# Optimization experiments

Hardware: AMD Instinct MI355X
Metric: run time of the kernel (lower is better)

Reference implementation:

```python
import jax, jax.numpy as jnp
import numpy as np

PRUNING_RATE = 0.1
ROPE_THETA = 10000.0
EPS = 1e-5


def _rms_norm(x, w):
    v = jnp.mean(jnp.square(x.astype(jnp.float32)), axis=-1, keepdims=True)
    return (x * jax.lax.rsqrt(v + EPS)).astype(x.dtype) * w


def _rotate_half(x):
    x1, x2 = jnp.split(x, 2, axis=-1)
    return jnp.concatenate([-x2, x1], axis=-1)


def setup_inputs() -> dict:
    key = jax.random.key(0)
    ks = jax.random.split(key, 11)
    B, Q, D, H, Dh, P, F = 2, 16, 2048, 16, 128, 8192, 5632
    K = P + Q
    s = D ** -0.5
    inp = {
        "hidden_states": jax.random.normal(ks[0], (B, Q, D), jnp.float32),
        "past_k": jax.random.normal(ks[1], (B, H, P, Dh), jnp.float32),
        "past_v": jax.random.normal(ks[2], (B, H, P, Dh), jnp.float32),
        "wq": jax.random.normal(ks[3], (D, D), jnp.float32) * s,
        "wk": jax.random.normal(ks[4], (D, D), jnp.float32) * s,
        "wv": jax.random.normal(ks[5], (D, D), jnp.float32) * s,
        "wo": jax.random.normal(ks[6], (D, D), jnp.float32) * s,
        "w_gate": jax.random.normal(ks[7], (D, F), jnp.float32) * s,
        "w_up": jax.random.normal(ks[8], (D, F), jnp.float32) * s,
        "w_down": jax.random.normal(ks[9], (F, D), jnp.float32) * (F ** -0.5),
        "norm1_w": jnp.ones((D,), jnp.float32),
        "norm2_w": jnp.ones((D,), jnp.float32),
    }
    # causal mask over [past + new] keys: query i (global pos P+i) sees keys <= P+i
    q_pos = P + jnp.arange(Q)
    k_pos = jnp.arange(K)
    mask = jnp.where(k_pos[None, :] <= q_pos[:, None], 0.0, -1e9).astype(jnp.float32)
    inp["attn_mask"] = jnp.broadcast_to(mask[None, None], (B, 1, Q, K))
    return inp


def reference(hidden_states, past_k, past_v, attn_mask, wq, wk, wv, wo,
              w_gate, w_up, w_down, norm1_w, norm2_w):
    B, Q, D = hidden_states.shape
    _, H, P, Dh = past_k.shape
    K = P + Q

    residual = hidden_states
    x = _rms_norm(hidden_states, norm1_w)
    q = (x @ wq).reshape(B, Q, H, Dh).transpose(0, 2, 1, 3)  # [B,H,Q,Dh]
    k = (x @ wk).reshape(B, Q, H, Dh).transpose(0, 2, 1, 3)
    v = (x @ wv).reshape(B, Q, H, Dh).transpose(0, 2, 1, 3)

    # RoPE at cache positions P..P+Q-1 (past keys already rotated)
    inv_freq = 1.0 / (ROPE_THETA ** (jnp.arange(0, Dh, 2, dtype=jnp.float32) / Dh))
    pos = (P + jnp.arange(Q)).astype(jnp.float32)
    emb = jnp.concatenate([pos[:, None] * inv_freq[None, :]] * 2, axis=-1)  # [Q,Dh]
    cos, sin = jnp.cos(emb), jnp.sin(emb)
    q = q * cos + _rotate_half(q) * sin
    k = k * cos + _rotate_half(k) * sin

    k_full = jnp.concatenate([past_k, k], axis=2)  # [B,H,K,Dh]
    v_full = jnp.concatenate([past_v, v], axis=2)

    scores = jnp.einsum("bhqd,bhkd->bhqk", q, k_full) / jnp.sqrt(jnp.float32(Dh))
    scores = scores + attn_mask
    attn = jax.nn.softmax(scores, axis=-1)  # eager weights (output_attentions=True)
    out = jnp.einsum("bhqk,bhkd->bhqd", attn, v_full)
    out = out.transpose(0, 2, 1, 3).reshape(B, Q, D) @ wo
    h = residual + out

    y = _rms_norm(h, norm2_w)
    new_hidden = h + (jax.nn.silu(y @ w_gate) * (y @ w_up)) @ w_down

    # importance-based KV eviction: mean attn to last query over batch*heads
    imp = jnp.sum(attn[:, :, Q - 1, :], axis=(0, 1)) / (B * H)  # [K]
    imp = imp.at[K - 1].set(jnp.inf)  # never evict the last token's key
    n_prune = int(PRUNING_RATE * K)
    _, prune_idxs = jax.lax.top_k(-imp, n_prune)  # smallest-importance keys
    return new_hidden, attn, prune_idxs
```

## Files before the change

### kernel.cpp

```cpp
#include <hip/hip_runtime.h>
#include <math.h>

#define BB 2
#define QQ 16
#define DD 2048
#define HH 16
#define DHH 128
#define PP 8192
#define FF 5632
#define KK 8208
#define BH 32
#define RR 32
#define NPRUNE 820

#define OFF_X      0u
#define OFF_QR     65536u
#define OFF_KN     131072u
#define OFF_VN     196608u
#define OFF_ROWM   262144u
#define OFF_ROWZ   262656u
#define OFF_OATTN  263168u
#define OFF_H      328704u
#define OFF_Y      394240u
#define OFF_ACT    459776u
#define OFF_UNION  640064u
#define OFF_P64P   (OFF_UNION + 12582912u)
#define OFF_F64    (OFF_P64P + 4456448u)
#define D_X64      0u
#define D_K64      65536u
#define D_Q64      131072u
#define D_M64      135168u
#define D_Z64      135200u
#define D_SC       135232u
#define D_KEYS     397888u
#define OFF_RANK   (OFF_F64 + 812192u)

__global__ __launch_bounds__(256) void rmsnorm_kernel(
    const float* __restrict__ in, const float* __restrict__ w,
    float* __restrict__ out)
{
    int r = blockIdx.x;
    const float* x = in + (size_t)r * DD;
    float ss = 0.f;
    for (int c = threadIdx.x; c < DD; c += 256) { float v = x[c]; ss = fmaf(v, v, ss); }
    __shared__ float red[256];
    red[threadIdx.x] = ss;
    __syncthreads();
    for (int off = 128; off > 0; off >>= 1) {
        if (threadIdx.x < off) red[threadIdx.x] += red[threadIdx.x + off];
        __syncthreads();
    }
    float mean = red[0] / (float)DD;
    float scale = 1.0f / sqrtf(mean + 1e-5f);
    for (int c = threadIdx.x; c < DD; c += 256)
        out[(size_t)r * DD + c] = x[c] * scale * w[c];
}

__global__ __launch_bounds__(256) void fused_rms_kernel(
    const float* __restrict__ in, const float* __restrict__ w,
    float* __restrict__ out32, double* __restrict__ out64)
{
    int bx = blockIdx.x, tid = threadIdx.x;
    __shared__ float red[256];
    __shared__ float bs[16];
    __shared__ float sscale;
    if (bx < 32) {
        int r = bx;
        const float* x = in + (size_t)r * DD;
        float ss = 0.f;
        for (int c = tid; c < DD; c += 256) { float v = x[c]; ss = fmaf(v, v, ss); }
        red[tid] = ss;
        __syncthreads();
        for (int off = 128; off > 0; off >>= 1) {
            if (tid < off) red[tid] += red[tid + off];
            __syncthreads();
        }
        float mean = red[0] / (float)DD;
        float scale = 1.0f / sqrtf(mean + 1e-5f);
        for (int c = tid; c < DD; c += 256)
            out32[(size_t)r * DD + c] = x[c] * scale * w[c];
    } else {
        int r = bx - 32;
        const float* x = in + (size_t)r * DD;
        if (tid < 16) {
            const float* a = x + tid * 128;
            float rr[8];
#pragma unroll
            for (int j = 0; j < 8; ++j) { float v = a[j]; rr[j] = __fmul_rn(v, v); }
            for (int i = 8; i < 128; i += 8) {
#pragma unroll
                for (int j = 0; j < 8; ++j) {
                    float v = a[i + j];
                    rr[j] = __fadd_rn(rr[j], __fmul_rn(v, v));
                }
            }
            float t01 = __fadd_rn(rr[0], rr[1]);
            float t23 = __fadd_rn(rr[2], rr[3]);
            float t45 = __fadd_rn(rr[4], rr[5]);
            float t67 = __fadd_rn(rr[6], rr[7]);
            bs[tid] = __fadd_rn(__fadd_rn(t01, t23), __fadd_rn(t45, t67));
        }
        __syncthreads();
        if (tid == 0) {
            float c[8], d[4], e[2];
#pragma unroll
            for (int i = 0; i < 8; ++i) c[i] = __fadd_rn(bs[2 * i], bs[2 * i + 1]);
#pragma unroll
            for (int i = 0; i < 4; ++i) d[i] = __fadd_rn(c[2 * i], c[2 * i + 1]);
            e[0] = __fadd_rn(d[0], d[1]);
            e[1] = __fadd_rn(d[2], d[3]);
            float s = __fadd_rn(e[0], e[1]);
            float v = __fdiv_rn(s, 2048.0f);
            float ve = __fadd_rn(v, 1e-5f);
            float sq = __fsqrt_rn(ve);
            sscale = __fdiv_rn(1.0f, sq);
        }
        __syncthreads();
        double scd = (double)sscale;
        for (int c = tid; c < DD; c += 256)
            out64[(size_t)r * DD + c] = ((double)x[c] * scd) * (double)w[c];
    }
}

template<int DCHUNK>
__global__ __launch_bounds__(256) void gemm32c2(
    const float* __restrict__ A, const float* __restrict__ w0,
    const float* __restrict__ w1, const float* __restrict__ w2,
    float* __restrict__ part, int Kdim, int N, size_t zstride)
{
    int cc = blockIdx.x, kc = blockIdx.y, z = blockIdx.z;
    int tid = threadIdx.x;
    int col0 = cc * 512 + tid;
    int d0 = kc * DCHUNK;
    const float* W = (z == 0) ? w0 : (z == 1) ? w1 : w2;
    __shared__ __align__(16) float xs[32 * DCHUNK];
    for (int i = tid; i < 32 * DCHUNK; i += 256) {
        int r = i / DCHUNK, d = i - r * DCHUNK;
        xs[i] = A[(size_t)r * Kdim + d0 + d];
    }
    __syncthreads();
    float acc0[32], acc1[32];
#pragma unroll
    for (int r = 0; r < 32; ++r) { acc0[r] = 0.f; acc1[r] = 0.f; }
    const float* wp = W + (size_t)d0 * N + col0;
    for (int d = 0; d < DCHUNK; d += 8) {
        float wb0[8], wb1[8];
#pragma unroll
        for (int u = 0; u < 8; ++u) {
            wb0[u] = wp[(size_t)(d + u) * N];
            wb1[u] = wp[(size_t)(d + u) * N + 256];
        }
#pragma unroll
        for (int r = 0; r < 32; ++r) {
            const float4 x0 = *(const float4*)(xs + r * DCHUNK + d);
            const float4 x1 = *(const float4*)(xs + r * DCHUNK + d + 4);
            float a = acc0[r], b = acc1[r];
            a = fmaf(x0.x, wb0[0], a);  b = fmaf(x0.x, wb1[0], b);
            a = fmaf(x0.y, wb0[1], a);  b = fmaf(x0.y, wb1[1], b);
            a = fmaf(x0.z, wb0[2], a);  b = fmaf(x0.z, wb1[2], b);
            a = fmaf(x0.w, wb0[3], a);  b = fmaf(x0.w, wb1[3], b);
            a = fmaf(x1.x, wb0[4], a);  b = fmaf(x1.x, wb1[4], b);
            a = fmaf(x1.y, wb0[5], a);  b = fmaf(x1.y, wb1[5], b);
            a = fmaf(x1.z, wb0[6], a);  b = fmaf(x1.z, wb1[6], b);
            a = fmaf(x1.w, wb0[7], a);  b = fmaf(x1.w, wb1[7], b);
            acc0[r] = a; acc1[r] = b;
        }
    }
    float* dst = part + (size_t)z * zstride;
#pragma unroll
    for (int r = 0; r < 32; ++r) {
        dst[((size_t)(kc * 32 + r)) * N + col0] = acc0[r];
        dst[((size_t)(kc * 32 + r)) * N + col0 + 256] = acc1[r];
    }
}

__global__ __launch_bounds__(256) void fused_qkv_p64_kernel(
    const float* __restrict__ A, const float* __restrict__ wq,
    const float* __restrict__ wk, const float* __restrict__ wv,
    float* __restrict__ part, const double* __restrict__ x64,
    double* __restrict__ p64)
{
    int bx = blockIdx.x, tid = threadIdx.x;
    __shared__ __align__(16) float xs[32 * 32];
    __shared__ double xs64[34 * 64];
    if (bx < 768) {
        int cc = bx & 3, kc = (bx >> 2) & 63, z = bx >> 8;
        int col0 = cc * 512 + tid;
        int d0 = kc * 32;
        const float* W = (z == 0) ? wq : (z == 1) ? wk : wv;
        for (int i = tid; i < 32 * 32; i += 256) {
            int r = i >> 5, d = i & 31;
            xs[i] = A[(size_t)r * DD + d0 + d];
        }
        __syncthreads();
        float acc0[32], acc1[32];
#pragma unroll
        for (int r = 0; r < 32; ++r) { acc0[r] = 0.f; acc1[r] = 0.f; }
        const float* wp = W + (size_t)d0 * DD + col0;
        for (int d = 0; d < 32; d += 8) {
            float wb0[8], wb1[8];
#pragma unroll
            for (int u = 0; u < 8; ++u) {
                wb0[u] = wp[(size_t)(d + u) * DD];
                wb1[u] = wp[(size_t)(d + u) * DD + 256];
            }
#pragma unroll
            for (int r = 0; r < 32; ++r) {
                const float4 x0 = *(const float4*)(xs + r * 32 + d);
                const float4 x1 = *(const float4*)(xs + r * 32 + d + 4);
                float a = acc0[r], b = acc1[r];
                a = fmaf(x0.x, wb0[0], a);  b = fmaf(x0.x, wb1[0], b);
                a = fmaf(x0.y, wb0[1], a);  b = fmaf(x0.y, wb1[1], b);
                a = fmaf(x0.z, wb0[2], a);  b = fmaf(x0.z, wb1[2], b);
                a = fmaf(x0.w, wb0[3], a);  b = fmaf(x0.w, wb1[3], b);
                a = fmaf(x1.x, wb0[4], a);  b = fmaf(x1.x, wb1[4], b);
                a = fmaf(x1.y, wb0[5], a);  b = fmaf(x1.y, wb1[5], b);
                a = fmaf(x1.z, wb0[6], a);  b = fmaf(x1.z, wb1[6], b);
                a = fmaf(x1.w, wb0[7], a);  b = fmaf(x1.w, wb1[7], b);
                acc0[r] = a; acc1[r] = b;
            }
        }
        float* dst = part + (size_t)z * 64 * 65536;
#pragma unroll
        for (int r = 0; r < 32; ++r) {
            dst[((size_t)(kc * 32 + r)) * DD + col0] = acc0[r];
            dst[((size_t)(kc * 32 + r)) * DD + col0 + 256] = acc1[r];
        }
    } else {
        int p = bx - 768;
        int cc = p & 7, kc = p >> 3;
        int col = cc * 256 + tid;
        int d0 = kc * 64;
        for (int i = tid; i < 34 * 64; i += 256) {
            int r = i >> 6, d = i & 63;
            int srcrow = (r < 32) ? r : ((r == 32) ? 15 : 31);
            xs64[i] = x64[(size_t)srcrow * DD + d0 + d];
        }
        __syncthreads();
        double acc[34];
#pragma unroll
        for (int r = 0; r < 34; ++r) acc[r] = 0.0;
        const float* wkp = wk + (size_t)d0 * DD + col;
        const float* wqp = wq + (size_t)d0 * DD + col;
        for (int d = 0; d < 64; d += 4) {
            double wkb[4], wqb[4];
#pragma unroll
            for (int u = 0; u < 4; ++u) {
                wkb[u] = (double)wkp[(size_t)(d + u) * DD];
                wqb[u] = (double)wqp[(size_t)(d + u) * DD];
            }
#pragma unroll
            for (int u = 0; u < 4; ++u) {
#pragma unroll
                for (int r = 0; r < 32; ++r) acc[r] = fma(xs64[r * 64 + d + u], wkb[u], acc[r]);
                acc[32] = fma(xs64[32 * 64 + d + u], wqb[u], acc[32]);
                acc[33] = fma(xs64[33 * 64 + d + u], wqb[u], acc[33]);
            }
        }
#pragma unroll
        for (int r = 0; r < 34; ++r)
            p64[((size_t)kc * 34 + r) * DD + col] = acc[r];
    }
}

__global__ __launch_bounds__(256) void fused_reduce_kernel(
    const float* __restrict__ part, float* __restrict__ qr,
    float* __restrict__ kn, float* __restrict__ vn,
    const double* __restrict__ p64, double* __restrict__ k64,
    double* __restrict__ q64)
{
    int bx = blockIdx.x, tid = threadIdx.x;
    __shared__ float buf[256];
    __shared__ double dbuf[256];
    if (bx < 256) {
        int r = bx >> 3;
        int b = r >> 4, qi = r & 15;
        int c = (bx & 7) * 256 + tid;
        int h = c >> 7, dh = c & 127, j = dh & 63;
        float invf = (float)exp(-((double)j / 64.0) * log(10000.0));
        float ang = (float)(PP + qi) * invf;
        float sn, cs;
        sincosf(ang, &sn, &cs);
        size_t dsti = (((size_t)(b * HH + h)) * QQ + qi) * DHH + dh;
        for (int mat = 0; mat < 3; ++mat) {
            const float* pm = part + (size_t)mat * 64 * 65536 + (size_t)r * DD + c;
            float sa = 0.f, sb = 0.f;
#pragma unroll 8
            for (int kc = 0; kc < 32; ++kc) {
                sa += pm[(size_t)kc * 32 * DD];
                sb += pm[(size_t)(kc + 32) * 32 * DD];
            }
            float s = sa + sb;
            buf[tid] = s;
            __syncthreads();
            float val;
            if (mat == 2) {
                val = s;
            } else {
                float other = (dh < 64) ? -buf[tid + 64] : buf[tid - 64];
                val = s * cs + other * sn;
            }
            float* dst = (mat == 0) ? qr : (mat == 1) ? kn : vn;
            dst[dsti] = val;
            __syncthreads();
        }
    } else {
        int e = (bx - 256) * 256 + tid;
        int r = e >> 11, col = e & 2047;
        double s = 0.0;
#pragma unroll 8
        for (int kc = 0; kc < 32; ++kc) s += p64[((size_t)kc * 34 + r) * DD + col];
        dbuf[tid] = s;
        __syncthreads();
        int dh = col & 127, j = dh & 63;
        int pos = (r < 32) ? (PP + (r & 15)) : (PP + 15);
        float pf = (float)pow(10000.0, (double)j / 64.0);
        float invf = __fdiv_rn(1.0f, pf);
        float ang = __fmul_rn((float)pos, invf);
        float cs = (float)cos((double)ang);
        float sn = (float)sin((double)ang);
        double outv;
        if (dh < 64) outv = s * (double)cs - dbuf[tid + 64] * (double)sn;
        else         outv = s * (double)cs + dbuf[tid - 64] * (double)sn;
        if (r < 32) k64[(size_t)r * DD + col] = outv;
        else        q64[(size_t)(r - 32) * DD + col] = outv;
    }
}

__global__ __launch_bounds__(256) void scores_kernel(
    const float* __restrict__ qr, const float* __restrict__ past_k,
    const float* __restrict__ kn, float* __restrict__ attn,
    const double* __restrict__ q64, const double* __restrict__ k64,
    double* __restrict__ sc64)
{
    int bh = blockIdx.x, ch = blockIdx.y;
    int b = bh >> 4, h = bh & 15;
    int tid = threadIdx.x;
    __shared__ __align__(16) float qs[QQ * DHH];
    __shared__ double q64s[DHH];
    for (int i = tid; i < QQ * DHH; i += 256) qs[i] = qr[(size_t)bh * (QQ * DHH) + i];
    if (tid < DHH) q64s[tid] = q64[(size_t)b * DD + h * DHH + tid];
    __syncthreads();

    if (ch < 16) {
        int kbase = ch * 512;
        const float* kr0 = past_k + ((size_t)bh * PP + kbase + tid) * DHH;
        float acc[2][QQ];
#pragma unroll
        for (int u = 0; u < 2; ++u)
#pragma unroll
            for (int q = 0; q < QQ; ++q) acc[u][q] = 0.f;
        double a64[2] = {0.0, 0.0};

        for (int jb = 0; jb < DHH / 4; jb += 2) {
            float4 kb[2][2];
#pragma unroll
            for (int u = 0; u < 2; ++u) {
                const float4* kp = (const float4*)(kr0 + (size_t)u * 256 * DHH);
                kb[u][0] = kp[jb];
                kb[u][1] = kp[jb + 1];
            }
#pragma unroll
            for (int jj = 0; jj < 2; ++jj) {
#pragma unroll
                for (int q = 0; q < QQ; ++q) {
                    float4 qv = *(const float4*)(qs + q * DHH + (jb + jj) * 4);
#pragma unroll
                    for (int u = 0; u < 2; ++u) {
                        acc[u][q] = fmaf(kb[u][jj].x, qv.x, acc[u][q]);
                        acc[u][q] = fmaf(kb[u][jj].y, qv.y, acc[u][q]);
                        acc[u][q] = fmaf(kb[u][jj].z, qv.z, acc[u][q]);
                        acc[u][q] = fmaf(kb[u][jj].w, qv.w, acc[u][q]);
                    }
                }
            }
#pragma unroll
            for (int jj = 0; jj < 2; ++jj) {
                int j = jb + jj;
#pragma unroll
                for (int u = 0; u < 2; ++u) {
                    a64[u] = fma((double)kb[u][jj].x, q64s[j * 4 + 0], a64[u]);
                    a64[u] = fma((double)kb[u][jj].y, q64s[j * 4 + 1], a64[u]);
                    a64[u] = fma((double)kb[u][jj].z, q64s[j * 4 + 2], a64[u]);
                    a64[u] = fma((double)kb[u][jj].w, q64s[j * 4 + 3], a64[u]);
                }
            }
        }
#pragma unroll
        for (int q = 0; q < QQ; ++q) {
#pragma unroll
            for (int u = 0; u < 2; ++u) {
                int key = kbase + u * 256 + tid;
                float sv = acc[u][q] / 11.313708498984761f;
                if (key > PP + q) sv += -1e9f;
                attn[((size_t)(bh * QQ + q)) * KK + key] = sv;
            }
        }
#pragma unroll
        for (int u = 0; u < 2; ++u)
            sc64[(size_t)bh * KK + kbase + u * 256 + tid] = a64[u] / (double)sqrtf(128.0f);
    } else {
        if (tid >= 16) return;
        const float* krow = kn + ((size_t)bh * QQ + tid) * DHH;
        float acc[QQ];
#pragma unroll
        for (int q = 0; q < QQ; ++q) acc[q] = 0.f;
        for (int j = 0; j < DHH / 4; ++j) {
            float4 kv = ((const float4*)krow)[j];
#pragma unroll
            for (int q = 0; q < QQ; ++q) {
                float4 qv = *(const float4*)(qs + q * DHH + j * 4);
                acc[q] = fmaf(kv.x, qv.x, acc[q]);
                acc[q] = fmaf(kv.y, qv.y, acc[q]);
                acc[q] = fmaf(kv.z, qv.z, acc[q]);
                acc[q] = fmaf(kv.w, qv.w, acc[q]);
            }
        }
        int key = PP + tid;
#pragma unroll
        for (int q = 0; q < QQ; ++q) {
            float sv = acc[q] / 11.313708498984761f;
            if (key > PP + q) sv += -1e9f;
            attn[((size_t)(bh * QQ + q)) * KK + key] = sv;
        }
        double a64 = 0.0;
        const double* kd = k64 + (size_t)(b * QQ + tid) * DD + h * DHH;
        for (int j = 0; j < DHH; ++j) a64 = fma(kd[j], q64s[j], a64);
        sc64[(size_t)bh * KK + key] = a64 / (double)sqrtf(128.0f);
    }
}

__global__ __launch_bounds__(256) void fused_rowstats_kernel(
    const float* __restrict__ attn, float* __restrict__ rowm, float* __restrict__ rowz,
    const double* __restrict__ sc, double* __restrict__ m64, double* __restrict__ z64)
{
    int bx = blockIdx.x, tid = threadIdx.x;
    __shared__ float sm[256], sz[256];
    __shared__ double dm[256], dz[256];
    if (bx < 512) {
        int row = bx;
        const float* s = attn + (size_t)row * KK;
        float m = -INFINITY, z = 0.f;
        for (int k = tid; k < KK; k += 256) {
            float v = s[k];
            float nm = fmaxf(m, v);
            z = z * expf(m - nm) + expf(v - nm);
            m = nm;
        }
        sm[tid] = m; sz[tid] = z;
        __syncthreads();
        for (int off = 128; off > 0; off >>= 1) {
            if (tid < off) {
                float m1 = sm[tid], z1 = sz[tid];
                float m2 = sm[tid + off], z2 = sz[tid + off];
                float nm = fmaxf(m1, m2);
                sm[tid] = nm;
                sz[tid] = z1 * expf(m1 - nm) + z2 * expf(m2 - nm);
            }
            __syncthreads();
        }
        if (tid == 0) { rowm[row] = sm[0]; rowz[row] = sz[0]; }
    } else {
        int row = bx - 512;
        const double* s = sc + (size_t)row * KK;
        double m = -INFINITY, z = 0.0;
        for (int k = tid; k < KK; k += 256) {
            double v = s[k];
            double nm = fmax(m, v);
            z = z * exp(m - nm) + exp(v - nm);
            m = nm;
        }
        dm[tid] = m; dz[tid] = z;
        __syncthreads();
        for (int off = 128; off > 0; off >>= 1) {
            if (tid < off) {
                double m1 = dm[tid], z1 = dz[tid];
                double m2 = dm[tid + off], z2 = dz[tid + off];
                double nm = fmax(m1, m2);
                dm[tid] = nm;
                dz[tid] = z1 * exp(m1 - nm) + z2 * exp(m2 - nm);
            }
            __syncthreads();
        }
        if (tid == 0) { m64[row] = dm[0]; z64[row] = dz[0]; }
    }
}

__global__ __launch_bounds__(256) void fused_pv_impkeys_kernel(
    float* __restrict__ attn, const float* __restrict__ past_v,
    const float* __restrict__ vn, const float* __restrict__ rowm,
    const float* __restrict__ rowz, float* __restrict__ part,
    const double* __restrict__ sc, const double* __restrict__ m64,
    const double* __restrict__ z64, unsigned long long* __restrict__ keys,
    int* __restrict__ rank)
{
    int bx = blockIdx.x, tid = threadIdx.x;
    __shared__ __align__(16) float p[QQ * 256];
    if (bx < 1056) {
        int bh = bx / 33, ch = bx - bh * 33;
        int nk = (ch < 32) ? 256 : 16;
        int kbase = ch * 256;
        if (tid < nk) {
            float sv[QQ];
#pragma unroll
            for (int q = 0; q < QQ; ++q)
                sv[q] = attn[((size_t)(bh * QQ + q)) * KK + kbase + tid];
#pragma unroll
            for (int q = 0; q < QQ; ++q) {
                int row = bh * QQ + q;
                float pv = expf(sv[q] - rowm[row]) / rowz[row];
                attn[((size_t)row) * KK + kbase + tid] = pv;
                p[q * 256 + tid] = pv;
            }
        }
        __syncthreads();

        int dq = tid & 31, q0 = tid >> 5;
        int d4 = dq * 4;
        float4 a0 = make_float4(0, 0, 0, 0), a1 = make_float4(0, 0, 0, 0);
        if (ch < 32) {
            const float* vbase = past_v + ((size_t)bh * PP + kbase) * DHH;
            for (int kk = 0; kk < 256; kk += 8) {
                float4 vb[8];
#pragma unroll
                for (int u = 0; u < 8; ++u)
                    vb[u] = *(const float4*)(vbase + (size_t)(kk + u) * DHH + d4);
#pragma unroll
                for (int u = 0; u < 8; ++u) {
                    float p0 = p[q0 * 256 + kk + u];
                    float p1 = p[(q0 + 8) * 256 + kk + u];
                    a0.x = fmaf(vb[u].x, p0, a0.x); a0.y = fmaf(vb[u].y, p0, a0.y);
                    a0.z = fmaf(vb[u].z, p0, a0.z); a0.w = fmaf(vb[u].w, p0, a0.w);
                    a1.x = fmaf(vb[u].x, p1, a1.x); a1.y = fmaf(vb[u].y, p1, a1.y);
                    a1.z = fmaf(vb[u].z, p1, a1.z); a1.w = fmaf(vb[u].w, p1, a1.w);
                }
            }
        } else {
            const float* vbase = vn + (size_t)bh * QQ * DHH;
            for (int kk = 0; kk < 16; ++kk) {
                float4 v4 = *(const float4*)(vbase + (size_t)kk * DHH + d4);
                float p0 = p[q0 * 256 + kk];
                float p1 = p[(q0 + 8) * 256 + kk];
                a0.x = fmaf(v4.x, p0, a0.x); a0.y = fmaf(v4.y, p0, a0.y);
                a0.z = fmaf(v4.z, p0, a0.z); a0.w = fmaf(v4.w, p0, a0.w);
                a1.x = fmaf(v4.x, p1, a1.x); a1.y = fmaf(v4.y, p1, a1.y);
                a1.z = fmaf(v4.z, p1, a1.z); a1.w = fmaf(v4.w, p1, a1.w);
            }
        }
        size_t pb = ((size_t)ch * BH + bh) * (QQ * DHH);
        *(float4*)(part + pb + q0 * DHH + d4) = a0;
        *(float4*)(part + pb + (q0 + 8) * DHH + d4) = a1;
    } else {
        int k = (bx - 1056) * 256 + tid;
        if (k >= KK) return;
        rank[k] = 0;
        double t = 0.0;
        for (int bh = 0; bh < BH; ++bh)
            t += exp(sc[(size_t)bh * KK + k] - m64[bh]) / z64[bh];
        double imp = t / 32.0;
        if (k == KK - 1) imp = INFINITY;
        unsigned long long bits = (unsigned long long)__double_as_longlong(imp);
        keys[k] = (bits & ~0x3FFFull) | (unsigned long long)k;
    }
}

__global__ __launch_bounds__(256) void fused_pvred_rankpart_kernel(
    const float* __restrict__ part, float* __restrict__ oattn,
    const unsigned long long* __restrict__ keys, int* __restrict__ rank)
{
    int bx = blockIdx.x, tid = threadIdx.x;
    __shared__ unsigned long long chnk[1026];
    if (bx < 256) {
        int e = bx * 256 + tid;
        float sa = 0.f, sb = 0.f;
#pragma unroll 8
        for (int ch = 0; ch < 16; ++ch) sa += part[(size_t)ch * 65536 + e];
#pragma unroll 8
        for (int ch = 16; ch < 33; ++ch) sb += part[(size_t)ch * 65536 + e];
        float s = sa + sb;
        int bh = e >> 11, rem = e & 2047, q = rem >> 7, d = rem & 127;
        int b = bh >> 4, h = bh & 15;
        oattn[((size_t)(b * QQ + q)) * DD + h * DHH + d] = s;
    } else {
        int idx = bx - 256;
        int xb = idx % 33, yb = idx / 33;
        int gid = xb * 256 + tid;
        int base = yb * 1026;
        for (int i = tid; i < 1026; i += 256) chnk[i] = keys[base + i];
        __syncthreads();
        if (gid >= KK) return;
        unsigned long long mykey = keys[gid];
        int cnt = 0;
#pragma unroll 6
        for (int i = 0; i < 1026; ++i) cnt += (chnk[i] < mykey) ? 1 : 0;
        atomicAdd(&rank[gid], cnt);
    }
}

__global__ __launch_bounds__(256) void fused_wogemm_rankwrite_kernel(
    const float* __restrict__ A, const float* __restrict__ wo,
    float* __restrict__ part,
    const unsigned long long* __restrict__ keys, const int* __restrict__ rank,
    float* __restrict__ outp)
{
    int bx = blockIdx.x, tid = threadIdx.x;
    __shared__ __align__(16) float xs[32 * 32];
    if (bx < 256) {
        int cc = bx & 3, kc = bx >> 2;
        int col0 = cc * 512 + tid;
        int d0 = kc * 32;
        for (int i = tid; i < 32 * 32; i += 256) {
            int r = i >> 5, d = i & 31;
            xs[i] = A[(size_t)r * DD + d0 + d];
        }
        __syncthreads();
        float acc0[32], acc1[32];
#pragma unroll
        for (int r = 0; r < 32; ++r) { acc0[r] = 0.f; acc1[r] = 0.f; }
        const float* wp = wo + (size_t)d0 * DD + col0;
        for (int d = 0; d < 32; d += 8) {
            float wb0[8], wb1[8];
#pragma unroll
            for (int u = 0; u < 8; ++u) {
                wb0[u] = wp[(size_t)(d + u) * DD];
                wb1[u] = wp[(size_t)(d + u) * DD + 256];
            }
#pragma unroll
            for (int r = 0; r < 32; ++r) {
                const float4 x0 = *(const float4*)(xs + r * 32 + d);
                const float4 x1 = *(const float4*)(xs + r * 32 + d + 4);
                float a = acc0[r], b = acc1[r];
                a = fmaf(x0.x, wb0[0], a);  b = fmaf(x0.x, wb1[0], b);
                a = fmaf(x0.y, wb0[1], a);  b = fmaf(x0.y, wb1[1], b);
                a = fmaf(x0.z, wb0[2], a);  b = fmaf(x0.z, wb1[2], b);
                a = fmaf(x0.w, wb0[3], a);  b = fmaf(x0.w, wb1[3], b);
                a = fmaf(x1.x, wb0[4], a);  b = fmaf(x1.x, wb1[4], b);
                a = fmaf(x1.y, wb0[5], a);  b = fmaf(x1.y, wb1[5], b);
                a = fmaf(x1.z, wb0[6], a);  b = fmaf(x1.z, wb1[6], b);
                a = fmaf(x1.w, wb0[7], a);  b = fmaf(x1.w, wb1[7], b);
                acc0[r] = a; acc1[r] = b;
            }
        }
#pragma unroll
        for (int r = 0; r < 32; ++r) {
            part[((size_t)(kc * 32 + r)) * DD + col0] = acc0[r];
            part[((size_t)(kc * 32 + r)) * DD + col0 + 256] = acc1[r];
        }
    } else {
        int gid = (bx - 256) * 256 + tid;
        if (gid >= KK) return;
        int r = rank[gid];
        if (r < NPRUNE)
            outp[r] = (float)(unsigned)(keys[gid] & 0x3FFFu);
    }
}

__global__ __launch_bounds__(256) void reduce_wo_kernel(
    const float* __restrict__ part, const float* __restrict__ resid,
    float* __restrict__ hbuf)
{
    int e = blockIdx.x * 256 + threadIdx.x;
    float sa = 0.f, sb = 0.f;
#pragma unroll 8
    for (int kc = 0; kc < 32; ++kc) {
        sa += part[(size_t)kc * 65536 + e];
        sb += part[(size_t)(kc + 32) * 65536 + e];
    }
    hbuf[e] = resid[e] + (sa + sb);
}

__global__ __launch_bounds__(256) void reduce_gateup_silu_kernel(
    const float* __restrict__ part, float* __restrict__ act)
{
    int e = blockIdx.x * 256 + threadIdx.x;
    float ga = 0.f, gb = 0.f, ua = 0.f, ub = 0.f;
#pragma unroll 8
    for (int kc = 0; kc < 16; ++kc) {
        ga += part[(size_t)kc * 180224 + e];
        gb += part[(size_t)(kc + 16) * 180224 + e];
        ua += part[(size_t)(kc + 32) * 180224 + e];
        ub += part[(size_t)(kc + 48) * 180224 + e];
    }
    float g = ga + gb, u = ua + ub;
    float sg = g / (1.f + expf(-g));
    act[e] = sg * u;
}

__global__ __launch_bounds__(256) void reduce_down_kernel(
    const float* __restrict__ part, const float* __restrict__ hbuf,
    float* __restrict__ out)
{
    int e = blockIdx.x * 256 + threadIdx.x;
    float sa = 0.f, sb = 0.f;
#pragma unroll 8
    for (int kc = 0; kc < 88; ++kc) {
        sa += part[(size_t)kc * 65536 + e];
        sb += part[(size_t)(kc + 88) * 65536 + e];
    }
    out[e] = hbuf[e] + (sa + sb);
}

extern "C" void kernel_launch(void* const* d_in, const int* in_sizes, int n_in,
                              void* d_out, int out_size, void* d_ws, size_t ws_size,
                              hipStream_t stream)
{
    const float* hidden = (const float*)d_in[0];
    const float* past_k = (const float*)d_in[1];
    const float* past_v = (const float*)d_in[2];
    const float* wq     = (const float*)d_in[3];
    const float* wk     = (const float*)d_in[4];
    const float* wv     = (const float*)d_in[5];
    const float* wo     = (const float*)d_in[6];
    const float* wgate  = (const float*)d_in[7];
    const float* wup    = (const float*)d_in[8];
    const float* wdown  = (const float*)d_in[9];
    const float* n1w    = (const float*)d_in[10];
    const float* n2w    = (const float*)d_in[11];

    float* out_hidden = (float*)d_out;
    float* attn = out_hidden + (size_t)RR * DD;
    float* out_prune = attn + (size_t)BH * QQ * KK;
    float* ws = (float*)d_ws;
    double* p64part = (double*)(ws + OFF_P64P);
    double* f64 = (double*)(ws + OFF_F64);
    double* x64 = f64 + D_X64;
    double* k64 = f64 + D_K64;
    double* q64 = f64 + D_Q64;
    double* m64 = f64 + D_M64;
    double* z64 = f64 + D_Z64;
    double* sc64 = f64 + D_SC;
    unsigned long long* keys = (unsigned long long*)(f64 + D_KEYS);
    int* rank = (int*)(ws + OFF_RANK);

    fused_rms_kernel<<<dim3(64), dim3(256), 0, stream>>>(hidden, n1w, ws + OFF_X, x64);

    fused_qkv_p64_kernel<<<dim3(1024), dim3(256), 0, stream>>>(
        ws + OFF_X, wq, wk, wv, ws + OFF_UNION, x64, p64part);

    fused_reduce_kernel<<<dim3(528), dim3(256), 0, stream>>>(
        ws + OFF_UNION, ws + OFF_QR, ws + OFF_KN, ws + OFF_VN, p64part, k64, q64);

    scores_kernel<<<dim3(BH, 17), dim3(256), 0, stream>>>(
        ws + OFF_QR, past_k, ws + OFF_KN, attn, q64, k64, sc64);

    fused_rowstats_kernel<<<dim3(544), dim3(256), 0, stream>>>(
        attn, ws + OFF_ROWM, ws + OFF_ROWZ, sc64, m64, z64);

    fused_pv_impkeys_kernel<<<dim3(1089), dim3(256), 0, stream>>>(
        attn, past_v, ws + OFF_VN, ws + OFF_ROWM, ws + OFF_ROWZ, ws + OFF_UNION,
        sc64, m64, z64, keys, rank);

    fused_pvred_rankpart_kernel<<<dim3(520), dim3(256), 0, stream>>>(
        ws + OFF_UNION, ws + OFF_OATTN, keys, rank);

    fused_wogemm_rankwrite_kernel<<<dim3(289), dim3(256), 0, stream>>>(
        ws + OFF_OATTN, wo, ws + OFF_UNION, keys, rank, out_prune);

    reduce_wo_kernel<<<dim3(256), dim3(256), 0, stream>>>(ws + OFF_UNION, hidden, ws + OFF_H);

    rmsnorm_kernel<<<dim3(RR), dim3(256), 0, stream>>>(ws + OFF_H, n2w, ws + OFF_Y);

    gemm32c2<64><<<dim3(11, 32, 2), dim3(256), 0, stream>>>(
        ws + OFF_Y, wgate, wup, wup, ws + OFF_UNION, DD, FF, (size_t)32 * 180224);
    reduce_gateup_silu_kernel<<<dim3(704), dim3(256), 0, stream>>>(
        ws + OFF_UNION, ws + OFF_ACT);

    gemm32c2<32><<<dim3(4, 176, 1), dim3(256), 0, stream>>>(
        ws + OFF_ACT, wdown, wdown, wdown, ws + OFF_UNION, FF, DD, 0);
    reduce_down_kernel<<<dim3(256), dim3(256), 0, stream>>>(
        ws + OFF_UNION, ws + OFF_H, out_hidden);
}
```

Before: 324.5 us.

## Fuse per-chunk softmax max/sum partials into scores kernel, shrink rowstats pass

The scores kernel now computes an online-softmax max and sum for each query row over its 512-key chunk, using wave shuffles plus a small shared-memory combine, and writes 17 partials per row. The fp32 branch of the rowstats kernel then merges those partials instead of re-reading the whole 512x8208 attention score matrix, so that branch drops from 512 blocks to 2. This removes a large global-memory read pass. In exchange, the scores kernel does 16 serialized block-level reductions, each with two __syncthreads, which lengthens its tail. The masking add is also dropped for past keys, which is valid because those keys are never masked.

Measured after the change: 344.6 us. +6.2%, slower.

```diff
diff --git a/kernel.cpp b/kernel.cpp
--- a/kernel.cpp
+++ b/kernel.cpp
@@ -34,6 +34,10 @@
 #define D_SC       135232u
 #define D_KEYS     397888u
 #define OFF_RANK   (OFF_F64 + 812192u)
+#define OFF_PMAX   (OFF_RANK + 8320u)
+#define OFF_PSUM   (OFF_PMAX + 8704u)
+
+#define SENT (-3.0e38f)
 
 __global__ __launch_bounds__(256) void rmsnorm_kernel(
     const float* __restrict__ in, const float* __restrict__ w,
@@ -331,17 +335,19 @@
     const float* __restrict__ qr, const float* __restrict__ past_k,
     const float* __restrict__ kn, float* __restrict__ attn,
     const double* __restrict__ q64, const double* __restrict__ k64,
-    double* __restrict__ sc64)
+    double* __restrict__ sc64, float* __restrict__ pmax, float* __restrict__ psum)
 {
     int bh = blockIdx.x, ch = blockIdx.y;
     int b = bh >> 4, h = bh & 15;
     int tid = threadIdx.x;
     __shared__ __align__(16) float qs[QQ * DHH];
     __shared__ double q64s[DHH];
+    __shared__ float swm[4], swz[4];
     for (int i = tid; i < QQ * DHH; i += 256) qs[i] = qr[(size_t)bh * (QQ * DHH) + i];
     if (tid < DHH) q64s[tid] = q64[(size_t)b * DD + h * DHH + tid];
     __syncthreads();
 
+    float lmq[QQ], lzq[QQ];
     if (ch < 16) {
         int kbase = ch * 512;
         const float* kr0 = past_k + ((size_t)bh * PP + kbase + tid) * DHH;
@@ -388,80 +394,102 @@
         }
 #pragma unroll
         for (int q = 0; q < QQ; ++q) {
-#pragma unroll
-            for (int u = 0; u < 2; ++u) {
-                int key = kbase + u * 256 + tid;
-                float sv = acc[u][q] / 11.313708498984761f;
-                if (key > PP + q) sv += -1e9f;
-                attn[((size_t)(bh * QQ + q)) * KK + key] = sv;
-            }
+            float sv0 = acc[0][q] / 11.313708498984761f;
+            float sv1 = acc[1][q] / 11.313708498984761f;
+            attn[((size_t)(bh * QQ + q)) * KK + kbase + tid] = sv0;
+            attn[((size_t)(bh * QQ + q)) * KK + kbase + 256 + tid] = sv1;
+            float lm = fmaxf(sv0, sv1);
+            lmq[q] = lm;
+            lzq[q] = expf(sv0 - lm) + expf(sv1 - lm);
         }
 #pragma unroll
         for (int u = 0; u < 2; ++u)
             sc64[(size_t)bh * KK + kbase + u * 256 + tid] = a64[u] / (double)sqrtf(128.0f);
     } else {
-        if (tid >= 16) return;
-        const float* krow = kn + ((size_t)bh * QQ + tid) * DHH;
-        float acc[QQ];
-#pragma unroll
-        for (int q = 0; q < QQ; ++q) acc[q] = 0.f;
-        for (int j = 0; j < DHH / 4; ++j) {
-            float4 kv = ((const float4*)krow)[j];
+#pragma unroll
+        for (int q = 0; q < QQ; ++q) { lmq[q] = SENT; lzq[q] = 0.f; }
+        if (tid < 16) {
+            const float* krow = kn + ((size_t)bh * QQ + tid) * DHH;
+            float acc[QQ];
+#pragma unroll
+            for (int q = 0; q < QQ; ++q) acc[q] = 0.f;
+            for (int j = 0; j < DHH / 4; ++j) {
+                float4 kv = ((const float4*)krow)[j];
+#pragma unroll
+                for (int q = 0; q < QQ; ++q) {
+                    float4 qv = *(const float4*)(qs + q * DHH + j * 4);
+                    acc[q] = fmaf(kv.x, qv.x, acc[q]);
+                    acc[q] = fmaf(kv.y, qv.y, acc[q]);
+                    acc[q] = fmaf(kv.z, qv.z, acc[q]);
+                    acc[q] = fmaf(kv.w, qv.w, acc[q]);
+                }
+            }
+            int key = PP + tid;
 #pragma unroll
             for (int q = 0; q < QQ; ++q) {
-                float4 qv = *(const float4*)(qs + q * DHH + j * 4);
-                acc[q] = fmaf(kv.x, qv.x, acc[q]);
-                acc[q] = fmaf(kv.y, qv.y, acc[q]);
-                acc[q] = fmaf(kv.z, qv.z, acc[q]);
-                acc[q] = fmaf(kv.w, qv.w, acc[q]);
-            }
-        }
-        int key = PP + tid;
-#pragma unroll
-        for (int q = 0; q < QQ; ++q) {
-            float sv = acc[q] / 11.313708498984761f;
-            if (key > PP + q) sv += -1e9f;
-            attn[((size_t)(bh * QQ + q)) * KK + key] = sv;
-        }
-        double a64 = 0.0;
-        const double* kd = k64 + (size_t)(b * QQ + tid) * DD + h * DHH;
-        for (int j = 0; j < DHH; ++j) a64 = fma(kd[j], q64s[j], a64);
-        sc64[(size_t)bh * KK + key] = a64 / (double)sqrtf(128.0f);
+                float sv = acc[q] / 11.313708498984761f;
+                if (key > PP + q) sv += -1e9f;
+                attn[((size_t)(bh * QQ + q)) * KK + key] = sv;
+                lmq[q] = sv;
+                lzq[q] = 1.f;
+            }
+            double a64 = 0.0;
+            const double* kd = k64 + (size_t)(b * QQ + tid) * DD + h * DHH;
+            for (int j = 0; j < DHH; ++j) a64 = fma(kd[j], q64s[j], a64);
+            sc64[(size_t)bh * KK + key] = a64 / (double)sqrtf(128.0f);
+        }
+    }
+
+    int wv = tid >> 6, ln = tid & 63;
+#pragma unroll 1
+    for (int q = 0; q < QQ; ++q) {
+        float lm = lmq[q], lz = lzq[q];
+        for (int off = 1; off < 64; off <<= 1) {
+            float om = __shfl_xor(lm, off, 64);
+            float oz = __shfl_xor(lz, off, 64);
+            float nm = fmaxf(lm, om);
+            lz = lz * expf(lm - nm) + oz * expf(om - nm);
+            lm = nm;
+        }
+        if (ln == 0) { swm[wv] = lm; swz[wv] = lz; }
+        __syncthreads();
+        if (tid == 0) {
+            float m = swm[0], z = swz[0];
+#pragma unroll
+            for (int w = 1; w < 4; ++w) {
+                float nm = fmaxf(m, swm[w]);
+                z = z * expf(m - nm) + swz[w] * expf(swm[w] - nm);
+                m = nm;
+            }
+            pmax[(size_t)(bh * QQ + q) * 17 + ch] = m;
+            psum[(size_t)(bh * QQ + q) * 17 + ch] = z;
+        }
+        __syncthreads();
     }
 }
 
 __global__ __launch_bounds__(256) void fused_rowstats_kernel(
-    const float* __restrict__ attn, float* __restrict__ rowm, float* __restrict__ rowz,
+    const float* __restrict__ pmax, const float* __restrict__ psum,
+    float* __restrict__ rowm, float* __restrict__ rowz,
     const double* __restrict__ sc, double* __restrict__ m64, double* __restrict__ z64)
 {
     int bx = blockIdx.x, tid = threadIdx.x;
-    __shared__ float sm[256], sz[256];
     __shared__ double dm[256], dz[256];
-    if (bx < 512) {
-        int row = bx;
-        const float* s = attn + (size_t)row * KK;
-        float m = -INFINITY, z = 0.f;
-        for (int k = tid; k < KK; k += 256) {
-            float v = s[k];
-            float nm = fmaxf(m, v);
-            z = z * expf(m - nm) + expf(v - nm);
+    if (bx < 2) {
+        int row = bx * 256 + tid;
+        float m = SENT, z = 0.f;
+#pragma unroll
+        for (int ch = 0; ch < 17; ++ch) {
+            float pm = pmax[(size_t)row * 17 + ch];
+            float pz = psum[(size_t)row * 17 + ch];
+            float nm = fmaxf(m, pm);
+            z = z * expf(m - nm) + pz * expf(pm - nm);
             m = nm;
         }
-        sm[tid] = m; sz[tid] = z;
-        __syncthreads();
-        for (int off = 128; off > 0; off >>= 1) {
-            if (tid < off) {
-                float m1 = sm[tid], z1 = sz[tid];
-                float m2 = sm[tid + off], z2 = sz[tid + off];
-                float nm = fmaxf(m1, m2);
-                sm[tid] = nm;
-                sz[tid] = z1 * expf(m1 - nm) + z2 * expf(m2 - nm);
-            }
-            __syncthreads();
-        }
-        if (tid == 0) { rowm[row] = sm[0]; rowz[row] = sz[0]; }
+        rowm[row] = m;
+        rowz[row] = z;
     } else {
-        int row = bx - 512;
+        int row = bx - 2;
         const double* s = sc + (size_t)row * KK;
         double m = -INFINITY, z = 0.0;
         for (int k = tid; k < KK; k += 256) {
@@ -731,6 +759,8 @@
     double* sc64 = f64 + D_SC;
     unsigned long long* keys = (unsigned long long*)(f64 + D_KEYS);
     int* rank = (int*)(ws + OFF_RANK);
+    float* pmax = ws + OFF_PMAX;
+    float* psum = ws + OFF_PSUM;
 
     fused_rms_kernel<<<dim3(64), dim3(256), 0, stream>>>(hidden, n1w, ws + OFF_X, x64);
 
@@ -741,10 +771,10 @@
         ws + OFF_UNION, ws + OFF_QR, ws + OFF_KN, ws + OFF_VN, p64part, k64, q64);
 
     scores_kernel<<<dim3(BH, 17), dim3(256), 0, stream>>>(
-        ws + OFF_QR, past_k, ws + OFF_KN, attn, q64, k64, sc64);
-
-    fused_rowstats_kernel<<<dim3(544), dim3(256), 0, stream>>>(
-        attn, ws + OFF_ROWM, ws + OFF_ROWZ, sc64, m64, z64);
+        ws + OFF_QR, past_k, ws + OFF_KN, attn, q64, k64, sc64, pmax, psum);
+
+    fused_rowstats_kernel<<<dim3(34), dim3(256), 0, stream>>>(
+        pmax, psum, ws + OFF_ROWM, ws + OFF_ROWZ, sc64, m64, z64);
 
     fused_pv_impkeys_kernel<<<dim3(1089), dim3(256), 0, stream>>>(
         attn, past_v, ws + OFF_VN, ws + OFF_ROWM, ws + OFF_ROWZ, ws + OFF_UNION,
```
